# Kernel tuning notes

Measured on AMD Instinct MI355X. Metric: run time of the kernel, lower is better.

Reference implementation:

```python
import jax, jax.numpy as jnp
import numpy as np

D = 6          # atom_dims, fixed by GroupNorm(2, D) and reshape(-1, 6)
K = 16         # neighbors
N_LAYERS = 3
C_IN = 2 * D + 1  # 13
EPS = 1e-5
SLOPE = 0.2


def _lrelu(x):
    return jnp.where(x >= 0, x, SLOPE * x)


def _group_norm(x, w, b):
    # x: [M, D], 2 groups of D//2 channels, affine per channel
    m = x.shape[0]
    xg = x.reshape(m, 2, D // 2)
    mu = xg.mean(-1, keepdims=True)
    var = xg.var(-1, keepdims=True)
    xn = ((xg - mu) * jax.lax.rsqrt(var + EPS)).reshape(m, D)
    return xn * w + b


def setup_inputs() -> dict:
    key = jax.random.key(0)
    ks = jax.random.split(key, 8)
    B, N = 4, 100000
    dist = jax.random.uniform(ks[0], (B, N, K, 1), dtype=jnp.float32)
    atomtypes = jax.random.uniform(ks[1], (B, N, K, D), dtype=jnp.float32)
    s1 = 1.0 / np.sqrt(C_IN)
    W1 = jax.random.uniform(ks[2], (N_LAYERS, C_IN, C_IN), jnp.float32, -s1, s1)
    b1 = jax.random.uniform(ks[3], (N_LAYERS, C_IN), jnp.float32, -s1, s1)
    W2 = jax.random.uniform(ks[4], (N_LAYERS, C_IN, D), jnp.float32, -s1, s1)
    b2 = jax.random.uniform(ks[5], (N_LAYERS, D), jnp.float32, -s1, s1)
    gw = jnp.ones((N_LAYERS, D), jnp.float32)
    gb = jnp.zeros((N_LAYERS, D), jnp.float32)
    return {"dist": dist, "atomtypes": atomtypes, "W1": W1, "b1": b1,
            "W2": W2, "b2": b2, "gw": gw, "gb": gb}


def reference(dist, atomtypes, W1, b1, W2, b2, gw, gb):
    B, N, k, d = atomtypes.shape
    point_emb = jnp.ones((B, N, d), dtype=atomtypes.dtype)
    for i in range(N_LAYERS):
        # [B,N,k,2D+1]: broadcast point emb to neighbors, concat atom feats + dist
        feat = jnp.concatenate(
            [jnp.broadcast_to(point_emb[:, :, None, :], (B, N, k, d)),
             atomtypes, dist], axis=-1)
        h = _lrelu(jnp.einsum('bnkc,cd->bnkd', feat, W1[i]) + b1[i])
        msg = (jnp.einsum('bnkc,cd->bnkd', h, W2[i]) + b2[i]).sum(-2)  # [B,N,D]
        upd = _lrelu(_group_norm(msg.reshape(-1, d), gw[i], gb[i])).reshape(B, N, d)
        point_emb = point_emb + upd
    return point_emb
```

## Files before the change

kernel.cpp:

```cpp
#include <hip/hip_runtime.h>


constexpr int DD  = 6;
constexpr int KK  = 16;
constexpr int CIN = 13;
constexpr float EPSV = 1e-5f;

__global__ __launch_bounds__(256) void atom_mp(
    const float* __restrict__ dist,
    const float* __restrict__ at,
    const float* __restrict__ W1,
    const float* __restrict__ b1,
    const float* __restrict__ W2,
    const float* __restrict__ b2,
    const float* __restrict__ gw,
    const float* __restrict__ gb,
    float* __restrict__ out,
    int P)
{
    const int p = blockIdx.x * blockDim.x + threadIdx.x;
    if (p >= P) return;

    const float* __restrict__ ab = at   + (long)p * (KK * DD);
    const float* __restrict__ db = dist + (long)p * KK;

    float pe[DD] = {1.f, 1.f, 1.f, 1.f, 1.f, 1.f};

    #pragma unroll 1
    for (int L = 0; L < 3; ++L) {
        const float* w1  = W1 + L * CIN * CIN;
        const float* w2  = W2 + L * CIN * DD;
        const float* bb1 = b1 + L * CIN;
        const float* bb2 = b2 + L * DD;
        const float* gwp = gw + L * DD;
        const float* gbp = gb + L * DD;

        float base[CIN];
        #pragma unroll
        for (int d = 0; d < CIN; ++d) base[d] = bb1[d];
        #pragma unroll
        for (int c = 0; c < DD; ++c) {
            const float pc = pe[c];
            #pragma unroll
            for (int d = 0; d < CIN; ++d)
                base[d] = fmaf(pc, w1[c * CIN + d], base[d]);
        }

        float hs1[CIN], hs2[CIN];
        #pragma unroll
        for (int d = 0; d < CIN; ++d) { hs1[d] = 0.f; hs2[d] = 0.f; }

        #pragma unroll
        for (int kp = 0; kp < 8; ++kp) {
            const float4* fp4 =
                reinterpret_cast<const float4*>(ab + kp * 12);
            const float4 q0 = fp4[0];
            const float4 q1 = fp4[1];
            const float4 q2 = fp4[2];
            const float2 dd2 =
                *reinterpret_cast<const float2*>(db + 2 * kp);

            const float f0[6] = {q0.x, q0.y, q0.z, q0.w, q1.x, q1.y};
            const float f1[6] = {q1.z, q1.w, q2.x, q2.y, q2.z, q2.w};

            float x0[CIN], x1[CIN];
            #pragma unroll
            for (int d = 0; d < CIN; ++d) { x0[d] = base[d]; x1[d] = base[d]; }

            #pragma unroll
            for (int j = 0; j < 6; ++j) {
                const float a0 = f0[j], a1 = f1[j];
                const float* wr = w1 + (6 + j) * CIN;
                #pragma unroll
                for (int d = 0; d < CIN; ++d) {
                    const float w = wr[d];
                    x0[d] = fmaf(a0, w, x0[d]);
                    x1[d] = fmaf(a1, w, x1[d]);
                }
            }
            {
                const float* wr = w1 + 12 * CIN;
                #pragma unroll
                for (int d = 0; d < CIN; ++d) {
                    const float w = wr[d];
                    x0[d] = fmaf(dd2.x, w, x0[d]);
                    x1[d] = fmaf(dd2.y, w, x1[d]);
                }
            }
            #pragma unroll
            for (int d = 0; d < CIN; ++d) {
                hs1[d] += x0[d];
                hs2[d] += __builtin_fabsf(x0[d]);
                hs1[d] += x1[d];
                hs2[d] += __builtin_fabsf(x1[d]);
            }
        }

        float hsum[CIN];
        #pragma unroll
        for (int d = 0; d < CIN; ++d)
            hsum[d] = fmaf(0.6f, hs1[d], 0.4f * hs2[d]);

        float msg[DD];
        #pragma unroll
        for (int d = 0; d < DD; ++d) msg[d] = 16.f * bb2[d];
        #pragma unroll
        for (int c = 0; c < CIN; ++c) {
            const float hc = hsum[c];
            #pragma unroll
            for (int d = 0; d < DD; ++d)
                msg[d] = fmaf(hc, w2[c * DD + d], msg[d]);
        }

        #pragma unroll
        for (int g = 0; g < 2; ++g) {
            float m0 = msg[3 * g], m1 = msg[3 * g + 1], m2 = msg[3 * g + 2];
            float mu = (m0 + m1 + m2) * (1.f / 3.f);
            float d0 = m0 - mu, d1 = m1 - mu, d2 = m2 - mu;
            float var = (d0 * d0 + d1 * d1 + d2 * d2) * (1.f / 3.f);
            float rs = rsqrtf(var + EPSV);
            float dv[3] = {d0, d1, d2};
            #pragma unroll
            for (int c = 0; c < 3; ++c) {
                int ch = 3 * g + c;
                float xn = fmaf(dv[c] * rs, gwp[ch], gbp[ch]);
                pe[ch] = fmaf(0.6f, xn, pe[ch]);
                pe[ch] = fmaf(0.4f, __builtin_fabsf(xn), pe[ch]);
            }
        }
    }

    float* op = out + (long)p * DD;
    *reinterpret_cast<float2*>(op)     = make_float2(pe[0], pe[1]);
    *reinterpret_cast<float2*>(op + 2) = make_float2(pe[2], pe[3]);
    *reinterpret_cast<float2*>(op + 4) = make_float2(pe[4], pe[5]);
}

extern "C" void kernel_launch(void* const* d_in, const int* in_sizes, int n_in,
                              void* d_out, int out_size, void* d_ws, size_t ws_size,
                              hipStream_t stream) {
    const float* dist = (const float*)d_in[0];
    const float* at   = (const float*)d_in[1];
    const float* W1   = (const float*)d_in[2];
    const float* b1   = (const float*)d_in[3];
    const float* W2   = (const float*)d_in[4];
    const float* b2   = (const float*)d_in[5];
    const float* gw   = (const float*)d_in[6];
    const float* gb   = (const float*)d_in[7];
    float* out = (float*)d_out;

    int P = in_sizes[0] / KK;
    int threads = 256;
    int blocks = (P + threads - 1) / threads;
    atom_mp<<<blocks, threads, 0, stream>>>(dist, at, W1, b1, W2, b2, gw, gb, out, P);
}
```

Measured before the change: 336.0 us.

## Split each point's neighbors across two lanes and combine partial sums via shuffle

Each point is now handled by two adjacent threads, each processing 8 of the 16 neighbors, with the per-channel hidden sums combined through a cross-lane xor shuffle before the second linear layer and group norm. This doubles the thread count to raise parallelism and latency hiding for the memory-bound neighbor reads. The per-neighbor compute is also restructured into a single fused chain per output channel, accumulating straight into the sums. The cost is that the base, second-layer and norm work is now computed redundantly in both lanes, plus the shuffles and split output stores.

```diff
diff --git a/kernel.cpp b/kernel.cpp
--- a/kernel.cpp
+++ b/kernel.cpp
@@ -4,9 +4,10 @@
 constexpr int DD  = 6;
 constexpr int KK  = 16;
 constexpr int CIN = 13;
+constexpr int TPB = 256;
 constexpr float EPSV = 1e-5f;
 
-__global__ __launch_bounds__(256) void atom_mp(
+__global__ __launch_bounds__(TPB) void atom_mp(
     const float* __restrict__ dist,
     const float* __restrict__ at,
     const float* __restrict__ W1,
@@ -18,11 +19,21 @@
     float* __restrict__ out,
     int P)
 {
-    const int p = blockIdx.x * blockDim.x + threadIdx.x;
+    const int t = blockIdx.x * TPB + threadIdx.x;
+    const int p = t >> 1;
+    const int h = t & 1;
     if (p >= P) return;
 
-    const float* __restrict__ ab = at   + (long)p * (KK * DD);
-    const float* __restrict__ db = dist + (long)p * KK;
+    const float* __restrict__ ab = at + (long)p * (KK * DD) + h * (8 * DD);
+
+    float dq[8];
+    {
+        const float4* dp4 = reinterpret_cast<const float4*>(
+            dist + (long)p * KK + h * 8);
+        float4 q0 = dp4[0], q1 = dp4[1];
+        dq[0] = q0.x; dq[1] = q0.y; dq[2] = q0.z; dq[3] = q0.w;
+        dq[4] = q1.x; dq[5] = q1.y; dq[6] = q1.z; dq[7] = q1.w;
+    }
 
     float pe[DD] = {1.f, 1.f, 1.f, 1.f, 1.f, 1.f};
 
@@ -41,9 +52,10 @@
         #pragma unroll
         for (int c = 0; c < DD; ++c) {
             const float pc = pe[c];
+            const float* wr = w1 + c * CIN;
             #pragma unroll
             for (int d = 0; d < CIN; ++d)
-                base[d] = fmaf(pc, w1[c * CIN + d], base[d]);
+                base[d] = fmaf(pc, wr[d], base[d]);
         }
 
         float hs1[CIN], hs2[CIN];
@@ -51,48 +63,64 @@
         for (int d = 0; d < CIN; ++d) { hs1[d] = 0.f; hs2[d] = 0.f; }
 
         #pragma unroll
-        for (int kp = 0; kp < 8; ++kp) {
-            const float4* fp4 =
-                reinterpret_cast<const float4*>(ab + kp * 12);
-            const float4 q0 = fp4[0];
-            const float4 q1 = fp4[1];
-            const float4 q2 = fp4[2];
-            const float2 dd2 =
-                *reinterpret_cast<const float2*>(db + 2 * kp);
+        for (int kp = 0; kp < 4; ++kp) {
+            const float4* fp4 = reinterpret_cast<const float4*>(ab + kp * 12);
+            const float4 A = fp4[0];
+            const float4 B = fp4[1];
+            const float4 C = fp4[2];
 
-            const float f0[6] = {q0.x, q0.y, q0.z, q0.w, q1.x, q1.y};
-            const float f1[6] = {q1.z, q1.w, q2.x, q2.y, q2.z, q2.w};
-
-            float x0[CIN], x1[CIN];
-            #pragma unroll
-            for (int d = 0; d < CIN; ++d) { x0[d] = base[d]; x1[d] = base[d]; }
-
-            #pragma unroll
-            for (int j = 0; j < 6; ++j) {
-                const float a0 = f0[j], a1 = f1[j];
-                const float* wr = w1 + (6 + j) * CIN;
+            {
+                const float f0 = A.x, f1 = A.y, f2 = A.z,
+                            f3 = A.w, f4 = B.x, f5 = B.y;
+                const float fd = dq[2 * kp];
+                float x[CIN];
+                #pragma unroll
+                for (int d = 0; d < CIN; ++d) x[d] = base[d];
+                const float* wr6  = w1 +  6 * CIN;
+                const float* wr7  = w1 +  7 * CIN;
+                const float* wr8  = w1 +  8 * CIN;
+                const float* wr9  = w1 +  9 * CIN;
+                const float* wr10 = w1 + 10 * CIN;
+                const float* wr11 = w1 + 11 * CIN;
+                const float* wr12 = w1 + 12 * CIN;
                 #pragma unroll
                 for (int d = 0; d < CIN; ++d) {
-                    const float w = wr[d];
-                    x0[d] = fmaf(a0, w, x0[d]);
-                    x1[d] = fmaf(a1, w, x1[d]);
+                    float xx = x[d];
+                    xx = fmaf(f0, wr6[d],  xx);
+                    xx = fmaf(f1, wr7[d],  xx);
+                    xx = fmaf(f2, wr8[d],  xx);
+                    xx = fmaf(f3, wr9[d],  xx);
+                    xx = fmaf(f4, wr10[d], xx);
+                    xx = fmaf(f5, wr11[d], xx);
+                    xx = fmaf(fd, wr12[d], xx);
+                    hs1[d] += xx;
+                    hs2[d] += __builtin_fabsf(xx);
                 }
             }
             {
-                const float* wr = w1 + 12 * CIN;
+                const float f0 = B.z, f1 = B.w, f2 = C.x,
+                            f3 = C.y, f4 = C.z, f5 = C.w;
+                const float fd = dq[2 * kp + 1];
+                const float* wr6  = w1 +  6 * CIN;
+                const float* wr7  = w1 +  7 * CIN;
+                const float* wr8  = w1 +  8 * CIN;
+                const float* wr9  = w1 +  9 * CIN;
+                const float* wr10 = w1 + 10 * CIN;
+                const float* wr11 = w1 + 11 * CIN;
+                const float* wr12 = w1 + 12 * CIN;
                 #pragma unroll
                 for (int d = 0; d < CIN; ++d) {
-                    const float w = wr[d];
-                    x0[d] = fmaf(dd2.x, w, x0[d]);
-                    x1[d] = fmaf(dd2.y, w, x1[d]);
+                    float xx = base[d];
+                    xx = fmaf(f0, wr6[d],  xx);
+                    xx = fmaf(f1, wr7[d],  xx);
+                    xx = fmaf(f2, wr8[d],  xx);
+                    xx = fmaf(f3, wr9[d],  xx);
+                    xx = fmaf(f4, wr10[d], xx);
+                    xx = fmaf(f5, wr11[d], xx);
+                    xx = fmaf(fd, wr12[d], xx);
+                    hs1[d] += xx;
+                    hs2[d] += __builtin_fabsf(xx);
                 }
-            }
-            #pragma unroll
-            for (int d = 0; d < CIN; ++d) {
-                hs1[d] += x0[d];
-                hs2[d] += __builtin_fabsf(x0[d]);
-                hs1[d] += x1[d];
-                hs2[d] += __builtin_fabsf(x1[d]);
             }
         }
 
@@ -100,6 +128,9 @@
         #pragma unroll
         for (int d = 0; d < CIN; ++d)
             hsum[d] = fmaf(0.6f, hs1[d], 0.4f * hs2[d]);
+        #pragma unroll
+        for (int d = 0; d < CIN; ++d)
+            hsum[d] += __shfl_xor(hsum[d], 1, 64);
 
         float msg[DD];
         #pragma unroll
@@ -107,9 +138,10 @@
         #pragma unroll
         for (int c = 0; c < CIN; ++c) {
             const float hc = hsum[c];
+            const float* wr = w2 + c * DD;
             #pragma unroll
             for (int d = 0; d < DD; ++d)
-                msg[d] = fmaf(hc, w2[c * DD + d], msg[d]);
+                msg[d] = fmaf(hc, wr[d], msg[d]);
         }
 
         #pragma unroll
@@ -131,9 +163,12 @@
     }
 
     float* op = out + (long)p * DD;
-    *reinterpret_cast<float2*>(op)     = make_float2(pe[0], pe[1]);
-    *reinterpret_cast<float2*>(op + 2) = make_float2(pe[2], pe[3]);
-    *reinterpret_cast<float2*>(op + 4) = make_float2(pe[4], pe[5]);
+    if (h == 0) {
+        *reinterpret_cast<float2*>(op)     = make_float2(pe[0], pe[1]);
+        *reinterpret_cast<float2*>(op + 2) = make_float2(pe[2], pe[3]);
+    } else {
+        *reinterpret_cast<float2*>(op + 4) = make_float2(pe[4], pe[5]);
+    }
 }
 
 extern "C" void kernel_launch(void* const* d_in, const int* in_sizes, int n_in,
@@ -150,7 +185,7 @@
     float* out = (float*)d_out;
 
     int P = in_sizes[0] / KK;
-    int threads = 256;
-    int blocks = (P + threads - 1) / threads;
-    atom_mp<<<blocks, threads, 0, stream>>>(dist, at, W1, b1, W2, b2, gw, gb, out, P);
+    long threads_total = 2L * P;
+    int blocks = (int)((threads_total + TPB - 1) / TPB);
+    atom_mp<<<blocks, TPB, 0, stream>>>(dist, at, W1, b1, W2, b2, gw, gb, out, P);
 }
```

After: 269.3 us. 19.9% less time.
